# Performance work log

Measured on AMD Instinct MI355X. Metric: run time of the kernel, lower is better.

## Reference

```python
import jax, jax.numpy as jnp
import numpy as np
from jax import lax

B, T, D = 64, 2048, 80
H = 128          # hidden_dim
H2 = 2 * H       # conv out channels / GRU input / bi-GRU output
L = 2            # gru layers
O = 4            # output_dim


def setup_inputs() -> dict:
    key = jax.random.key(0)
    ks = jax.random.split(key, 16)
    f = lambda k, shape, scale: (jax.random.normal(k, shape) * scale).astype(jnp.float32)
    return {
        "x": f(ks[0], (B, T, D), 1.0),
        # conv branches: PyTorch Conv1d weight layout [out, in, k]
        "conv1_w": f(ks[1], (H2, D, 1), 0.1), "conv1_b": f(ks[2], (H2,), 0.1),
        "conv3_w": f(ks[3], (H2, D, 3), 0.06), "conv3_b": f(ks[4], (H2,), 0.1),
        "conv5_w": f(ks[5], (H2, D, 5), 0.05), "conv5_b": f(ks[6], (H2,), 0.1),
        # skip / head linears: PyTorch Linear weight layout [out, in]
        "fc1_w": f(ks[7], (H2, D), 0.1), "fc1_b": f(ks[8], (H2,), 0.1),
        "fc_w": f(ks[9], (O, H2), 0.06), "fc_b": f(ks[10], (O,), 0.1),
        # stacked bidirectional GRU weights: [layer, dir(0=fwd,1=bwd), 3H, ...]
        # gate order along 3H axis follows PyTorch: reset, update, new
        "gru_wih": f(ks[11], (L, 2, 3 * H, H2), 0.06),
        "gru_whh": f(ks[12], (L, 2, 3 * H, H), 0.08),
        "gru_bih": f(ks[13], (L, 2, 3 * H), 0.05),
        "gru_bhh": f(ks[14], (L, 2, 3 * H), 0.05),
    }


def _conv_relu(xc, w, b, pad):
    # xc: [B, C, T], w: [out, in, k]
    y = lax.conv_general_dilated(xc, w, window_strides=(1,), padding=[(pad, pad)],
                                 dimension_numbers=("NCH", "OIH", "NCH"))
    return jax.nn.relu(y + b[None, :, None])


def _gru_dir(xin, wih, whh, bih, bhh, reverse):
    # xin: [B, T, Din]; PyTorch GRU cell: r,z,n gate order
    Hd = whh.shape[1]
    xg = jnp.einsum("btd,gd->btg", xin, wih) + bih  # [B, T, 3H]
    if reverse:
        xg = xg[:, ::-1]

    def step(h, xt):
        hg = h @ whh.T + bhh                                   # [B, 3H]
        r = jax.nn.sigmoid(xt[:, :Hd] + hg[:, :Hd])
        z = jax.nn.sigmoid(xt[:, Hd:2 * Hd] + hg[:, Hd:2 * Hd])
        n = jnp.tanh(xt[:, 2 * Hd:] + r * hg[:, 2 * Hd:])
        hn = (1.0 - z) * n + z * h
        return hn, hn

    h0 = jnp.zeros((xin.shape[0], Hd), xin.dtype)
    _, hs = lax.scan(step, h0, xg.transpose(1, 0, 2))          # [T, B, H]
    hs = hs.transpose(1, 0, 2)
    return hs[:, ::-1] if reverse else hs


def reference(x, conv1_w, conv1_b, conv3_w, conv3_b, conv5_w, conv5_b,
              fc1_w, fc1_b, fc_w, fc_b, gru_wih, gru_whh, gru_bih, gru_bhh):
    xc = x.transpose(0, 2, 1)                                   # [B, D, T]
    oc = (_conv_relu(xc, conv1_w, conv1_b, 0)
          + _conv_relu(xc, conv3_w, conv3_b, 1)
          + _conv_relu(xc, conv5_w, conv5_b, 2))                # [B, 2H, T]
    h = oc.transpose(0, 2, 1)                                   # [B, T, 2H]

    for l in range(gru_wih.shape[0]):
        fwd = _gru_dir(h, gru_wih[l, 0], gru_whh[l, 0], gru_bih[l, 0], gru_bhh[l, 0], False)
        bwd = _gru_dir(h, gru_wih[l, 1], gru_whh[l, 1], gru_bih[l, 1], gru_bhh[l, 1], True)
        h = jnp.concatenate([fwd, bwd], axis=-1)                # [B, T, 2H]

    output_gru = h + x @ fc1_w.T + fc1_b                        # skip connection
    out = output_gru @ fc_w.T + fc_b                            # [B, T, O]
    return output_gru, out
```

## Files before the change

### kernel.cpp

```cpp
#include <hip/hip_runtime.h>
#include <hip/hip_bf16.h>
#include <hip/hip_fp16.h>

typedef _Float16 f16;
typedef _Float16 h2_t __attribute__((ext_vector_type(2)));
typedef _Float16 h4_t __attribute__((ext_vector_type(4)));
typedef _Float16 h8_t __attribute__((ext_vector_type(8)));
typedef float    f4_t __attribute__((ext_vector_type(4)));

#define B_  64
#define T_  2048
#define BT_ 131072
#define OG_ELEMS 33554432ull

__device__ __forceinline__ void gl_lds16(const void* g, void* lds) {
  __builtin_amdgcn_global_load_lds(
      (const __attribute__((address_space(1))) void*)g,
      (__attribute__((address_space(3))) void*)lds, 16, 0, 0);
}

__device__ __forceinline__ h8_t pack8(const float* p) {
  f4_t a = *(const f4_t*)p;
  f4_t b = *(const f4_t*)(p + 4);
  return h8_t{(f16)a[0], (f16)a[1], (f16)a[2], (f16)a[3],
              (f16)b[0], (f16)b[1], (f16)b[2], (f16)b[3]};
}

__device__ __forceinline__ float dpp_swap1(float x) {
  int i = __builtin_bit_cast(int, x);
  int y = __builtin_amdgcn_update_dpp(0, i, 0xB1, 0xF, 0xF, true);
  return __builtin_bit_cast(float, y);
}

__device__ __forceinline__ void kloop128(
    const f16* __restrict__ Ab, int lda,
    const f16* __restrict__ Bb, int ldb,
    int ksteps, f16* As, f16* Bs, f4_t (&acc)[4][4])
{
  const int tid  = threadIdx.x;
  const int wave = tid >> 6, lane = tid & 63;
  const int srow = tid >> 2;
  const int scol = (tid & 3) * 8;
  const int fr   = lane & 15;
  const int kb   = (lane >> 4) * 8;
  const int rA   = (wave >> 1) * 64 + fr;
  const int rB   = (wave & 1) * 64 + fr;

  f16* dA0 = As + wave * 512;
  f16* dA1 = As + 2048 + wave * 512;
  f16* dB0 = Bs + wave * 512;
  f16* dB1 = Bs + 2048 + wave * 512;
  const f16* gA0 = Ab + (size_t)srow * lda + scol;
  const f16* gA1 = Ab + (size_t)(srow + 64) * lda + scol;
  const f16* gB0 = Bb + (size_t)srow * ldb + scol;
  const f16* gB1 = Bb + (size_t)(srow + 64) * ldb + scol;

  for (int kt = 0; kt < ksteps; ++kt) {
    const int ko = kt * 32;
    gl_lds16(gA0 + ko, dA0);
    gl_lds16(gA1 + ko, dA1);
    gl_lds16(gB0 + ko, dB0);
    gl_lds16(gB1 + ko, dB1);
    __syncthreads();
    h8_t af[4], bf[4];
#pragma unroll
    for (int m = 0; m < 4; m++) af[m] = *(const h8_t*)(As + (rA + m * 16) * 32 + kb);
#pragma unroll
    for (int n = 0; n < 4; n++) bf[n] = *(const h8_t*)(Bs + (rB + n * 16) * 32 + kb);
#pragma unroll
    for (int m = 0; m < 4; m++)
#pragma unroll
      for (int n = 0; n < 4; n++)
        acc[m][n] = __builtin_amdgcn_mfma_f32_16x16x32_f16(af[m], bf[n], acc[m][n], 0, 0, 0);
    __syncthreads();
  }
}

__global__ __launch_bounds__(256) void gemm_xT_kernel(
    const f16* __restrict__ A, int lda,
    const f16* __restrict__ Bw, int ldb,
    const float* __restrict__ bias,
    f16* __restrict__ out, int ksteps, int mode)
{
  __shared__ f16 As[4096];
  __shared__ f16 Bs[4096];
  f4_t acc[4][4];
#pragma unroll
  for (int m = 0; m < 4; m++)
#pragma unroll
    for (int n = 0; n < 4; n++) acc[m][n] = f4_t{0.f, 0.f, 0.f, 0.f};

  const f16* Ab = A + (size_t)blockIdx.x * 128 * lda;
  const f16* Bb = Bw + (size_t)blockIdx.y * 128 * ldb;
  kloop128(Ab, lda, Bb, ldb, ksteps, As, Bs, acc);

  const int tid = threadIdx.x, wave = tid >> 6, lane = tid & 63;
  const int col0 = blockIdx.y * 128 + (wave & 1) * 64 + (lane & 15);
  const int row0 = blockIdx.x * 128 + (wave >> 1) * 64 + (lane >> 4) * 4;
  const int b = blockIdx.x >> 4;
#pragma unroll
  for (int n = 0; n < 4; n++) {
    const int col = col0 + n * 16;
    const float bv = bias[col];
    const int g = col >> 7, jj = col & 127;
    const size_t base = (mode == 0)
        ? ((size_t)((b * 3 + g) * 128 + jj)) * 2048
        : ((size_t)((g * 64 + b) * 128 + jj)) * 2048;
#pragma unroll
    for (int m = 0; m < 4; m++) {
      const int row = row0 + m * 16;
      const int t = row & 2047;
      h4_t v = h4_t{(f16)(acc[m][n][0] + bv), (f16)(acc[m][n][1] + bv),
                    (f16)(acc[m][n][2] + bv), (f16)(acc[m][n][3] + bv)};
      *(h4_t*)(out + base + t) = v;
    }
  }
}

__global__ __launch_bounds__(256) void conv3sum_kernel(
    const f16* __restrict__ A5,
    const f16* __restrict__ W5p, const f16* __restrict__ W3p, const f16* __restrict__ W1p,
    const float* __restrict__ b5, const float* __restrict__ b3, const float* __restrict__ b1,
    f16* __restrict__ oc)
{
  __shared__ f16 As[4096];
  __shared__ f16 Bs[4096];
  const int tid = threadIdx.x, wave = tid >> 6, lane = tid & 63;
  const int col0 = blockIdx.y * 128 + (wave & 1) * 64 + (lane & 15);
  const int row0 = blockIdx.x * 128 + (wave >> 1) * 64 + (lane >> 4) * 4;
  const f16* Ab = A5 + (size_t)blockIdx.x * 128 * 480;

  f4_t tot[4][4];
#pragma unroll
  for (int m = 0; m < 4; m++)
#pragma unroll
    for (int n = 0; n < 4; n++) tot[m][n] = f4_t{0.f, 0.f, 0.f, 0.f};

  auto seg = [&](const f16* Wp, int ldb, int ks, int aoff, const float* bias) {
    f4_t acc[4][4];
#pragma unroll
    for (int m = 0; m < 4; m++)
#pragma unroll
      for (int n = 0; n < 4; n++) acc[m][n] = f4_t{0.f, 0.f, 0.f, 0.f};
    kloop128(Ab + aoff, 480, Wp + (size_t)blockIdx.y * 128 * ldb, ldb, ks, As, Bs, acc);
#pragma unroll
    for (int n = 0; n < 4; n++) {
      const float bv = bias[col0 + n * 16];
#pragma unroll
      for (int m = 0; m < 4; m++)
#pragma unroll
        for (int q = 0; q < 4; q++)
          tot[m][n][q] += fmaxf(acc[m][n][q] + bv, 0.f);
    }
  };
  seg(W5p, 480, 15, 0,   b5);
  seg(W3p, 288, 9,  96,  b3);
  seg(W1p, 96,  3,  192, b1);

#pragma unroll
  for (int n = 0; n < 4; n++) {
    const int col = col0 + n * 16;
#pragma unroll
    for (int m = 0; m < 4; m++) {
      const int row = row0 + m * 16;
#pragma unroll
      for (int q = 0; q < 4; q++)
        oc[(size_t)(row + q) * 256 + col] = (f16)tot[m][n][q];
    }
  }
}

__global__ __launch_bounds__(384) void im2col_kernel(
    const float* __restrict__ x, f16* __restrict__ A5)
{
  const int tid = threadIdx.x;
  const int r = tid / 12, c8 = tid % 12;
  const int bt = blockIdx.x * 32 + r;
  const int kg = blockIdx.y;
  const int b = bt >> 11, t = bt & 2047;
  const int ts = t + kg - 2;
  h8_t v = {0, 0, 0, 0, 0, 0, 0, 0};
  if (c8 < 10 && (unsigned)ts < 2048u) {
    const float* src = x + ((size_t)(b << 11) + ts) * 80 + c8 * 8;
    f4_t a = *(const f4_t*)src;
    f4_t bvec = *(const f4_t*)(src + 4);
    v = h8_t{(f16)a[0], (f16)a[1], (f16)a[2], (f16)a[3],
             (f16)bvec[0], (f16)bvec[1], (f16)bvec[2], (f16)bvec[3]};
  }
  *(h8_t*)(A5 + (size_t)bt * 480 + kg * 96 + c8 * 8) = v;
}

__global__ void pack_convw_kernel(
    const float* __restrict__ w1, const float* __restrict__ w3,
    const float* __restrict__ w5, const float* __restrict__ fc1w,
    f16* __restrict__ W5p, f16* __restrict__ W3p, f16* __restrict__ W1p,
    f16* __restrict__ FC1p)
{
  const int col = blockIdx.x;
  const int c = threadIdx.x;
  if (col < 480) {
    const int kg = col / 96, d = col % 96;
    W5p[c * 480 + col] = (f16)((d < 80) ? w5[(c * 80 + d) * 5 + kg] : 0.f);
  } else if (col < 768) {
    const int cc = col - 480, k = cc / 96, d = cc % 96;
    W3p[c * 288 + cc] = (f16)((d < 80) ? w3[(c * 80 + d) * 3 + k] : 0.f);
  } else if (col < 864) {
    const int d = col - 768;
    W1p[c * 96 + d] = (f16)((d < 80) ? w1[c * 80 + d] : 0.f);
  } else {
    const int d = col - 864;
    FC1p[c * 96 + d] = (f16)((d < 80) ? fc1w[c * 80 + d] : 0.f);
  }
}

__global__ void cast_f16_kernel(const float* __restrict__ src, f16* __restrict__ dst, int n8)
{
  const int i = blockIdx.x * blockDim.x + threadIdx.x;
  if (i >= n8) return;
  f4_t a = *(const f4_t*)(src + (size_t)i * 8);
  f4_t b = *(const f4_t*)(src + (size_t)i * 8 + 4);
  h8_t v = h8_t{(f16)a[0], (f16)a[1], (f16)a[2], (f16)a[3],
                (f16)b[0], (f16)b[1], (f16)b[2], (f16)b[3]};
  *(h8_t*)(dst + (size_t)i * 8) = v;
}

__device__ __forceinline__ float fastrcp(float x)  { return __builtin_amdgcn_rcpf(x); }
__device__ __forceinline__ float fastex2(float x)  { return __builtin_amdgcn_exp2f(x); }

#define DOT8(acc0, acc1, hv, wv)                                                       \
  do {                                                                                 \
    acc0 = __builtin_amdgcn_fdot2(h2_t{hv[0], hv[1]}, h2_t{wv[0], wv[1]}, acc0, false);\
    acc1 = __builtin_amdgcn_fdot2(h2_t{hv[2], hv[3]}, h2_t{wv[2], wv[3]}, acc1, false);\
    acc0 = __builtin_amdgcn_fdot2(h2_t{hv[4], hv[5]}, h2_t{wv[4], wv[5]}, acc0, false);\
    acc1 = __builtin_amdgcn_fdot2(h2_t{hv[6], hv[7]}, h2_t{wv[6], wv[7]}, acc1, false);\
  } while (0)

template<int DIR, int L1>
__device__ __forceinline__ void gru_chain(
    const f16* __restrict__ xg_b,
    const f16* __restrict__ xf_b,
    const f16* __restrict__ whh_d,
    const float* __restrict__ bhh_d,
    f16* __restrict__ h0_b,
    float* __restrict__ og_b)
{
  const int tid  = threadIdx.x;
  const int wv   = tid >> 6;
  const int lane = tid & 63;
  const int j    = wv * 32 + (lane >> 1);
  const int kh   = lane & 1;

  h8_t WR[8], WZ[8], WN[8];
  {
    const int co = kh * 64;
#pragma unroll
    for (int q = 0; q < 8; q++) WR[q] = *(const h8_t*)(whh_d + (size_t)j * 128 + co + q * 8);
#pragma unroll
    for (int q = 0; q < 8; q++) WZ[q] = *(const h8_t*)(whh_d + (size_t)(128 + j) * 128 + co + q * 8);
#pragma unroll
    for (int q = 0; q < 8; q++) WN[q] = *(const h8_t*)(whh_d + (size_t)(256 + j) * 128 + co + q * 8);
  }
#pragma unroll
  for (int q = 0; q < 8; q++) {
    asm volatile("" : "+v"(WR[q]), "+v"(WZ[q]), "+v"(WN[q]));
  }
  float br = bhh_d[j], bz = bhh_d[128 + j], bn = bhh_d[256 + j];
  asm volatile("" : "+v"(br), "+v"(bz), "+v"(bn));

  __shared__ __align__(16) f16 hb[2][128];
  if (tid < 128) { hb[0][tid] = (f16)0.f; hb[1][tid] = (f16)0.f; }
  float hstate = 0.f;

  h8_t xrA{}, xzA{}, xnA{}, xfA{};
  h8_t xrB{}, xzB{}, xnB{}, xfB{};
  auto ld4 = [&](int s8, h8_t& xr, h8_t& xz, h8_t& xn, h8_t& xf) {
    const int tb = DIR ? (T_ - 8 - s8) : s8;
    xr = *(const h8_t*)(xg_b + (size_t)(0 * 128 + j) * 2048 + tb);
    xz = *(const h8_t*)(xg_b + (size_t)(1 * 128 + j) * 2048 + tb);
    xn = *(const h8_t*)(xg_b + (size_t)(2 * 128 + j) * 2048 + tb);
    if (L1) xf = *(const h8_t*)(xf_b + (size_t)j * 2048 + tb);
  };
  ld4(0, xrA, xzA, xnA, xfA);
  asm volatile("s_waitcnt lgkmcnt(0)" ::: "memory");
  __builtin_amdgcn_s_barrier();
  __builtin_amdgcn_sched_barrier(0);

  for (int s8 = 0; s8 < T_; s8 += 8) {
    if ((s8 + 8) < T_) ld4(s8 + 8, xrB, xzB, xnB, xfB);
#pragma unroll
    for (int ss = 0; ss < 8; ss++) {
      const int e = DIR ? (7 - ss) : ss;
      const f16* hbuf = &hb[ss & 1][0] + kh * 64;
      h8_t hv[8];
#pragma unroll
      for (int q = 0; q < 8; q++) hv[q] = *(const h8_t*)(hbuf + q * 8);
      float r0 = 0.f, r1 = 0.f, z0 = 0.f, z1 = 0.f, n0 = 0.f, n1 = 0.f;
#pragma unroll
      for (int q = 0; q < 8; q++) {
        DOT8(r0, r1, hv[q], WR[q]);
        DOT8(z0, z1, hv[q], WZ[q]);
        DOT8(n0, n1, hv[q], WN[q]);
      }
      float sr = r0 + r1; sr += dpp_swap1(sr);
      float sz = z0 + z1; sz += dpp_swap1(sz);
      float sn = n0 + n1; sn += dpp_swap1(sn);
      const float rr = fastrcp(1.f + fastex2(((float)xrA[e] + sr + br) * -1.44269504f));
      const float zz = fastrcp(1.f + fastex2(((float)xzA[e] + sz + bz) * -1.44269504f));
      const float na = (float)xnA[e] + rr * (sn + bn);
      const float ex = fastex2(fabsf(na) * 2.88539008f);
      const float th = copysignf(1.f - 2.f * fastrcp(ex + 1.f), na);
      hstate = (1.f - zz) * th + zz * hstate;
      const int t = DIR ? (T_ - 1 - (s8 + ss)) : (s8 + ss);
      if (!kh) {
        if (L1) og_b[(size_t)t * 256 + j] = hstate + (float)xfA[e];
        else    h0_b[(size_t)t * 256 + j] = (f16)hstate;
        hb[(ss & 1) ^ 1][j] = (f16)hstate;
      }
      asm volatile("s_waitcnt lgkmcnt(0)" ::: "memory");
      __builtin_amdgcn_s_barrier();
      __builtin_amdgcn_sched_barrier(0);
    }
    xrA = xrB; xzA = xzB; xnA = xnB;
    if (L1) xfA = xfB;
  }
}

__global__ __launch_bounds__(256, 1) void gru_rec7_kernel(
    const f16* __restrict__ xgT, const f16* __restrict__ whhp,
    const float* __restrict__ bhh, const f16* __restrict__ xfT,
    f16* __restrict__ h0out, float* __restrict__ ogout)
{
  const int b = blockIdx.x >> 1, d = blockIdx.x & 1;
  const f16* xg_b = xgT + (size_t)(d * 64 + b) * 3 * 128 * 2048;
  const f16* xf_b = xfT ? (xfT + (size_t)(d * 64 + b) * 128 * 2048) : nullptr;
  const f16* whh_d = whhp + (size_t)d * 384 * 128;
  const float* bhh_d = bhh + d * 384;
  f16* h0_b = h0out ? (h0out + (size_t)b * 2048 * 256 + d * 128) : nullptr;
  float* og_b = ogout ? (ogout + (size_t)b * 2048 * 256 + d * 128) : nullptr;

  if (ogout) {
    if (d == 0) gru_chain<0, 1>(xg_b, xf_b, whh_d, bhh_d, nullptr, og_b);
    else        gru_chain<1, 1>(xg_b, xf_b, whh_d, bhh_d, nullptr, og_b);
  } else {
    if (d == 0) gru_chain<0, 0>(xg_b, nullptr, whh_d, bhh_d, h0_b, nullptr);
    else        gru_chain<1, 0>(xg_b, nullptr, whh_d, bhh_d, h0_b, nullptr);
  }
}

__global__ __launch_bounds__(256) void fc_out_kernel(
    const float* __restrict__ og, const float* __restrict__ fcw,
    const float* __restrict__ fcb, float* __restrict__ out)
{
  const int lane = threadIdx.x & 63;
  const int wid = (blockIdx.x * 256 + threadIdx.x) >> 6;
  const int nw = (gridDim.x * 256) >> 6;
  const f4_t w0 = *(const f4_t*)(fcw + 0 * 256 + lane * 4);
  const f4_t w1 = *(const f4_t*)(fcw + 1 * 256 + lane * 4);
  const f4_t w2 = *(const f4_t*)(fcw + 2 * 256 + lane * 4);
  const f4_t w3 = *(const f4_t*)(fcw + 3 * 256 + lane * 4);
  const float b0 = fcb[0], b1 = fcb[1], b2 = fcb[2], b3 = fcb[3];
  for (int row = wid; row < BT_; row += nw) {
    const f4_t v = *(const f4_t*)(og + (size_t)row * 256 + lane * 4);
    float p0 = v[0] * w0[0] + v[1] * w0[1] + v[2] * w0[2] + v[3] * w0[3];
    float p1 = v[0] * w1[0] + v[1] * w1[1] + v[2] * w1[2] + v[3] * w1[3];
    float p2 = v[0] * w2[0] + v[1] * w2[1] + v[2] * w2[2] + v[3] * w2[3];
    float p3 = v[0] * w3[0] + v[1] * w3[1] + v[2] * w3[2] + v[3] * w3[3];
#pragma unroll
    for (int off = 1; off < 64; off <<= 1) {
      p0 += __shfl_xor(p0, off);
      p1 += __shfl_xor(p1, off);
      p2 += __shfl_xor(p2, off);
      p3 += __shfl_xor(p3, off);
    }
    if (lane == 0) {
      f4_t o4 = f4_t{p0 + b0, p1 + b1, p2 + b2, p3 + b3};
      *(f4_t*)(out + (size_t)row * 4) = o4;
    }
  }
}

extern "C" void kernel_launch(void* const* d_in, const int* in_sizes, int n_in,
                              void* d_out, int out_size, void* d_ws, size_t ws_size,
                              hipStream_t stream)
{
  const float* x       = (const float*)d_in[0];
  const float* conv1_w = (const float*)d_in[1];
  const float* conv1_b = (const float*)d_in[2];
  const float* conv3_w = (const float*)d_in[3];
  const float* conv3_b = (const float*)d_in[4];
  const float* conv5_w = (const float*)d_in[5];
  const float* conv5_b = (const float*)d_in[6];
  const float* fc1_w   = (const float*)d_in[7];
  const float* fc1_b   = (const float*)d_in[8];
  const float* fc_w    = (const float*)d_in[9];
  const float* fc_b    = (const float*)d_in[10];
  const float* gru_wih = (const float*)d_in[11];
  const float* gru_whh = (const float*)d_in[12];
  const float* gru_bih = (const float*)d_in[13];
  const float* gru_bhh = (const float*)d_in[14];

  size_t off = 0;
  auto alloc = [&](size_t bytes) {
    char* p = (char*)d_ws + off;
    off += (bytes + 255) & ~(size_t)255;
    return p;
  };
  f16* A5   = (f16*)alloc((size_t)BT_ * 480 * 2);
  f16* W5p  = (f16*)alloc(256 * 480 * 2);
  f16* W3p  = (f16*)alloc(256 * 288 * 2);
  f16* W1p  = (f16*)alloc(256 * 96 * 2);
  f16* FC1p = (f16*)alloc(256 * 96 * 2);
  f16* wihp = (f16*)alloc(4ull * 384 * 256 * 2);
  f16* whhp = (f16*)alloc(4ull * 384 * 128 * 2);
  f16* oc   = (f16*)alloc((size_t)BT_ * 256 * 2);
  f16* xgT  = (f16*)alloc(2ull * 64 * 3 * 128 * 2048 * 2);
  f16* h0   = (f16*)alloc((size_t)BT_ * 256 * 2);
  f16* xfT  = (f16*)alloc(2ull * 64 * 128 * 2048 * 2);
  if (off > ws_size) return;

  float* og   = (float*)d_out;
  float* out2 = (float*)d_out + OG_ELEMS;

  im2col_kernel<<<dim3(BT_ / 32, 5), 384, 0, stream>>>(x, A5);
  pack_convw_kernel<<<960, 256, 0, stream>>>(conv1_w, conv3_w, conv5_w, fc1_w,
                                             W5p, W3p, W1p, FC1p);
  cast_f16_kernel<<<(49152 + 255) / 256, 256, 0, stream>>>(gru_wih, wihp, 49152);
  cast_f16_kernel<<<(24576 + 255) / 256, 256, 0, stream>>>(gru_whh, whhp, 24576);

  conv3sum_kernel<<<dim3(1024, 2), 256, 0, stream>>>(A5, W5p, W3p, W1p,
                                                     conv5_b, conv3_b, conv1_b, oc);
  gemm_xT_kernel<<<dim3(1024, 2), 256, 0, stream>>>(A5 + 192, 480, FC1p, 96,
                                                    fc1_b, xfT, 3, 1);

  for (int l = 0; l < 2; ++l) {
    const f16* hin = l ? h0 : oc;
    for (int d = 0; d < 2; ++d) {
      gemm_xT_kernel<<<dim3(1024, 3), 256, 0, stream>>>(
          hin, 256, wihp + (size_t)(l * 2 + d) * 384 * 256, 256,
          gru_bih + (l * 2 + d) * 384,
          xgT + (size_t)d * 64 * 3 * 128 * 2048, 8, 0);
    }
    gru_rec7_kernel<<<128, 256, 0, stream>>>(
        xgT, whhp + (size_t)l * 2 * 384 * 128, gru_bhh + (size_t)l * 2 * 384,
        l ? xfT : nullptr, l ? nullptr : h0, l ? og : nullptr);
  }

  fc_out_kernel<<<1024, 256, 0, stream>>>(og, fc_w, fc_b, out2);
}
```

Before: 2.185 ms.

## Process two batch sequences per GRU recurrence block to share barriers

The recurrent GRU kernel now has each workgroup advance two independent batch sequences in lockstep with shared register-resident weights. This halves the grid to 64 blocks. The aim is to amortize per-timestep LDS barrier and latency overhead across two chains and give the scheduler independent work to interleave. The cost is double the arithmetic per step on the serial path and fewer active CUs.

```diff
diff --git a/kernel.cpp b/kernel.cpp
--- a/kernel.cpp
+++ b/kernel.cpp
@@ -236,114 +236,156 @@
   } while (0)
 
 template<int DIR, int L1>
-__device__ __forceinline__ void gru_chain(
-    const f16* __restrict__ xg_b,
-    const f16* __restrict__ xf_b,
+__device__ __forceinline__ void gru_chain8(
+    const f16* __restrict__ xgA, const f16* __restrict__ xgB,
+    const f16* __restrict__ xfA_, const f16* __restrict__ xfB_,
     const f16* __restrict__ whh_d,
     const float* __restrict__ bhh_d,
-    f16* __restrict__ h0_b,
-    float* __restrict__ og_b)
+    f16* __restrict__ h0A, f16* __restrict__ h0B,
+    float* __restrict__ ogA, float* __restrict__ ogB)
 {
   const int tid  = threadIdx.x;
   const int wv   = tid >> 6;
   const int lane = tid & 63;
   const int j    = wv * 32 + (lane >> 1);
   const int kh   = lane & 1;
+  const int co   = kh * 64;
 
   h8_t WR[8], WZ[8], WN[8];
-  {
-    const int co = kh * 64;
-#pragma unroll
-    for (int q = 0; q < 8; q++) WR[q] = *(const h8_t*)(whh_d + (size_t)j * 128 + co + q * 8);
-#pragma unroll
-    for (int q = 0; q < 8; q++) WZ[q] = *(const h8_t*)(whh_d + (size_t)(128 + j) * 128 + co + q * 8);
-#pragma unroll
-    for (int q = 0; q < 8; q++) WN[q] = *(const h8_t*)(whh_d + (size_t)(256 + j) * 128 + co + q * 8);
-  }
-#pragma unroll
-  for (int q = 0; q < 8; q++) {
-    asm volatile("" : "+v"(WR[q]), "+v"(WZ[q]), "+v"(WN[q]));
-  }
-  float br = bhh_d[j], bz = bhh_d[128 + j], bn = bhh_d[256 + j];
-  asm volatile("" : "+v"(br), "+v"(bz), "+v"(bn));
-
-  __shared__ __align__(16) f16 hb[2][128];
-  if (tid < 128) { hb[0][tid] = (f16)0.f; hb[1][tid] = (f16)0.f; }
-  float hstate = 0.f;
-
-  h8_t xrA{}, xzA{}, xnA{}, xfA{};
-  h8_t xrB{}, xzB{}, xnB{}, xfB{};
-  auto ld4 = [&](int s8, h8_t& xr, h8_t& xz, h8_t& xn, h8_t& xf) {
+#pragma unroll
+  for (int q = 0; q < 8; q++) WR[q] = *(const h8_t*)(whh_d + (size_t)j * 128 + co + q * 8);
+#pragma unroll
+  for (int q = 0; q < 8; q++) WZ[q] = *(const h8_t*)(whh_d + (size_t)(128 + j) * 128 + co + q * 8);
+#pragma unroll
+  for (int q = 0; q < 8; q++) WN[q] = *(const h8_t*)(whh_d + (size_t)(256 + j) * 128 + co + q * 8);
+  const float br = bhh_d[j], bz = bhh_d[128 + j], bn = bhh_d[256 + j];
+
+  __shared__ __align__(16) f16 hbA[2][128];
+  __shared__ __align__(16) f16 hbB[2][128];
+  if (tid < 128) {
+    hbA[0][tid] = (f16)0.f; hbA[1][tid] = (f16)0.f;
+    hbB[0][tid] = (f16)0.f; hbB[1][tid] = (f16)0.f;
+  }
+  float hsA = 0.f, hsB = 0.f;
+
+  h8_t xrA0{}, xzA0{}, xnA0{}, xfA0{}, xrA1{}, xzA1{}, xnA1{}, xfA1{};
+  h8_t xrB0{}, xzB0{}, xnB0{}, xfB0{}, xrB1{}, xzB1{}, xnB1{}, xfB1{};
+  auto ld4 = [&](const f16* xg_b, const f16* xf_b, int s8,
+                 h8_t& xr, h8_t& xz, h8_t& xn, h8_t& xf) {
     const int tb = DIR ? (T_ - 8 - s8) : s8;
     xr = *(const h8_t*)(xg_b + (size_t)(0 * 128 + j) * 2048 + tb);
     xz = *(const h8_t*)(xg_b + (size_t)(1 * 128 + j) * 2048 + tb);
     xn = *(const h8_t*)(xg_b + (size_t)(2 * 128 + j) * 2048 + tb);
     if (L1) xf = *(const h8_t*)(xf_b + (size_t)j * 2048 + tb);
   };
-  ld4(0, xrA, xzA, xnA, xfA);
+  ld4(xgA, xfA_, 0, xrA0, xzA0, xnA0, xfA0);
+  ld4(xgB, xfB_, 0, xrB0, xzB0, xnB0, xfB0);
   asm volatile("s_waitcnt lgkmcnt(0)" ::: "memory");
   __builtin_amdgcn_s_barrier();
   __builtin_amdgcn_sched_barrier(0);
 
   for (int s8 = 0; s8 < T_; s8 += 8) {
-    if ((s8 + 8) < T_) ld4(s8 + 8, xrB, xzB, xnB, xfB);
+#pragma unroll
+    for (int q = 0; q < 8; q++) {
+      asm volatile("" : "+v"(WR[q]), "+v"(WZ[q]), "+v"(WN[q]));
+    }
+    if ((s8 + 8) < T_) {
+      ld4(xgA, xfA_, s8 + 8, xrA1, xzA1, xnA1, xfA1);
+      ld4(xgB, xfB_, s8 + 8, xrB1, xzB1, xnB1, xfB1);
+    }
 #pragma unroll
     for (int ss = 0; ss < 8; ss++) {
       const int e = DIR ? (7 - ss) : ss;
-      const f16* hbuf = &hb[ss & 1][0] + kh * 64;
-      h8_t hv[8];
-#pragma unroll
-      for (int q = 0; q < 8; q++) hv[q] = *(const h8_t*)(hbuf + q * 8);
-      float r0 = 0.f, r1 = 0.f, z0 = 0.f, z1 = 0.f, n0 = 0.f, n1 = 0.f;
+      const int t = DIR ? (T_ - 1 - (s8 + ss)) : (s8 + ss);
+      const f16* hbufA = &hbA[ss & 1][0] + co;
+      const f16* hbufB = &hbB[ss & 1][0] + co;
+      h8_t hvA[8], hvB[8];
+#pragma unroll
+      for (int q = 0; q < 8; q++) hvA[q] = *(const h8_t*)(hbufA + q * 8);
+#pragma unroll
+      for (int q = 0; q < 8; q++) hvB[q] = *(const h8_t*)(hbufB + q * 8);
+      float rA0 = 0.f, rA1 = 0.f, zA0 = 0.f, zA1 = 0.f, nA0 = 0.f, nA1 = 0.f;
 #pragma unroll
       for (int q = 0; q < 8; q++) {
-        DOT8(r0, r1, hv[q], WR[q]);
-        DOT8(z0, z1, hv[q], WZ[q]);
-        DOT8(n0, n1, hv[q], WN[q]);
+        DOT8(rA0, rA1, hvA[q], WR[q]);
+        DOT8(zA0, zA1, hvA[q], WZ[q]);
+        DOT8(nA0, nA1, hvA[q], WN[q]);
       }
-      float sr = r0 + r1; sr += dpp_swap1(sr);
-      float sz = z0 + z1; sz += dpp_swap1(sz);
-      float sn = n0 + n1; sn += dpp_swap1(sn);
-      const float rr = fastrcp(1.f + fastex2(((float)xrA[e] + sr + br) * -1.44269504f));
-      const float zz = fastrcp(1.f + fastex2(((float)xzA[e] + sz + bz) * -1.44269504f));
-      const float na = (float)xnA[e] + rr * (sn + bn);
-      const float ex = fastex2(fabsf(na) * 2.88539008f);
-      const float th = copysignf(1.f - 2.f * fastrcp(ex + 1.f), na);
-      hstate = (1.f - zz) * th + zz * hstate;
-      const int t = DIR ? (T_ - 1 - (s8 + ss)) : (s8 + ss);
-      if (!kh) {
-        if (L1) og_b[(size_t)t * 256 + j] = hstate + (float)xfA[e];
-        else    h0_b[(size_t)t * 256 + j] = (f16)hstate;
-        hb[(ss & 1) ^ 1][j] = (f16)hstate;
+      float rB0 = 0.f, rB1 = 0.f, zB0 = 0.f, zB1 = 0.f, nB0 = 0.f, nB1 = 0.f;
+#pragma unroll
+      for (int q = 0; q < 8; q++) {
+        DOT8(rB0, rB1, hvB[q], WR[q]);
+        DOT8(zB0, zB1, hvB[q], WZ[q]);
+        DOT8(nB0, nB1, hvB[q], WN[q]);
+      }
+      float srA = rA0 + rA1; srA += dpp_swap1(srA);
+      float szA = zA0 + zA1; szA += dpp_swap1(szA);
+      float snA = nA0 + nA1; snA += dpp_swap1(snA);
+      {
+        const float rr = fastrcp(1.f + fastex2(((float)xrA0[e] + srA + br) * -1.44269504f));
+        const float zz = fastrcp(1.f + fastex2(((float)xzA0[e] + szA + bz) * -1.44269504f));
+        const float na = (float)xnA0[e] + rr * (snA + bn);
+        const float ex = fastex2(fabsf(na) * 2.88539008f);
+        const float th = copysignf(1.f - 2.f * fastrcp(ex + 1.f), na);
+        hsA = (1.f - zz) * th + zz * hsA;
+        if (!kh) {
+          if (L1) ogA[(size_t)t * 256 + j] = hsA + (float)xfA0[e];
+          else    h0A[(size_t)t * 256 + j] = (f16)hsA;
+          hbA[(ss & 1) ^ 1][j] = (f16)hsA;
+        }
+      }
+      float srB = rB0 + rB1; srB += dpp_swap1(srB);
+      float szB = zB0 + zB1; szB += dpp_swap1(szB);
+      float snB = nB0 + nB1; snB += dpp_swap1(snB);
+      {
+        const float rr = fastrcp(1.f + fastex2(((float)xrB0[e] + srB + br) * -1.44269504f));
+        const float zz = fastrcp(1.f + fastex2(((float)xzB0[e] + szB + bz) * -1.44269504f));
+        const float na = (float)xnB0[e] + rr * (snB + bn);
+        const float ex = fastex2(fabsf(na) * 2.88539008f);
+        const float th = copysignf(1.f - 2.f * fastrcp(ex + 1.f), na);
+        hsB = (1.f - zz) * th + zz * hsB;
+        if (!kh) {
+          if (L1) ogB[(size_t)t * 256 + j] = hsB + (float)xfB0[e];
+          else    h0B[(size_t)t * 256 + j] = (f16)hsB;
+          hbB[(ss & 1) ^ 1][j] = (f16)hsB;
+        }
       }
       asm volatile("s_waitcnt lgkmcnt(0)" ::: "memory");
       __builtin_amdgcn_s_barrier();
       __builtin_amdgcn_sched_barrier(0);
     }
-    xrA = xrB; xzA = xzB; xnA = xnB;
-    if (L1) xfA = xfB;
-  }
-}
-
-__global__ __launch_bounds__(256, 1) void gru_rec7_kernel(
+    xrA0 = xrA1; xzA0 = xzA1; xnA0 = xnA1;
+    xrB0 = xrB1; xzB0 = xzB1; xnB0 = xnB1;
+    if (L1) { xfA0 = xfA1; xfB0 = xfB1; }
+  }
+}
+
+__global__ __launch_bounds__(256, 1) void gru_rec8_kernel(
     const f16* __restrict__ xgT, const f16* __restrict__ whhp,
     const float* __restrict__ bhh, const f16* __restrict__ xfT,
     f16* __restrict__ h0out, float* __restrict__ ogout)
 {
-  const int b = blockIdx.x >> 1, d = blockIdx.x & 1;
-  const f16* xg_b = xgT + (size_t)(d * 64 + b) * 3 * 128 * 2048;
-  const f16* xf_b = xfT ? (xfT + (size_t)(d * 64 + b) * 128 * 2048) : nullptr;
+  const int d  = blockIdx.x & 1;
+  const int bp = blockIdx.x >> 1;
+  const int bA = 2 * bp, bB = 2 * bp + 1;
+
+  const f16* xgA = xgT + (size_t)(d * 64 + bA) * 786432;
+  const f16* xgB = xgT + (size_t)(d * 64 + bB) * 786432;
+  const f16* xfA = xfT ? (xfT + (size_t)(d * 64 + bA) * 262144) : nullptr;
+  const f16* xfB = xfT ? (xfT + (size_t)(d * 64 + bB) * 262144) : nullptr;
   const f16* whh_d = whhp + (size_t)d * 384 * 128;
   const float* bhh_d = bhh + d * 384;
-  f16* h0_b = h0out ? (h0out + (size_t)b * 2048 * 256 + d * 128) : nullptr;
-  float* og_b = ogout ? (ogout + (size_t)b * 2048 * 256 + d * 128) : nullptr;
+  f16* h0A = h0out ? (h0out + (size_t)bA * 524288 + d * 128) : nullptr;
+  f16* h0B = h0out ? (h0out + (size_t)bB * 524288 + d * 128) : nullptr;
+  float* ogA = ogout ? (ogout + (size_t)bA * 524288 + d * 128) : nullptr;
+  float* ogB = ogout ? (ogout + (size_t)bB * 524288 + d * 128) : nullptr;
 
   if (ogout) {
-    if (d == 0) gru_chain<0, 1>(xg_b, xf_b, whh_d, bhh_d, nullptr, og_b);
-    else        gru_chain<1, 1>(xg_b, xf_b, whh_d, bhh_d, nullptr, og_b);
+    if (d == 0) gru_chain8<0, 1>(xgA, xgB, xfA, xfB, whh_d, bhh_d, nullptr, nullptr, ogA, ogB);
+    else        gru_chain8<1, 1>(xgA, xgB, xfA, xfB, whh_d, bhh_d, nullptr, nullptr, ogA, ogB);
   } else {
-    if (d == 0) gru_chain<0, 0>(xg_b, nullptr, whh_d, bhh_d, h0_b, nullptr);
-    else        gru_chain<1, 0>(xg_b, nullptr, whh_d, bhh_d, h0_b, nullptr);
+    if (d == 0) gru_chain8<0, 0>(xgA, xgB, nullptr, nullptr, whh_d, bhh_d, h0A, h0B, nullptr, nullptr);
+    else        gru_chain8<1, 0>(xgA, xgB, nullptr, nullptr, whh_d, bhh_d, h0A, h0B, nullptr, nullptr);
   }
 }
 
@@ -440,7 +482,7 @@
           gru_bih + (l * 2 + d) * 384,
           xgT + (size_t)d * 64 * 3 * 128 * 2048, 8, 0);
     }
-    gru_rec7_kernel<<<128, 256, 0, stream>>>(
+    gru_rec8_kernel<<<64, 256, 0, stream>>>(
         xgT, whhp + (size_t)l * 2 * 384 * 128, gru_bhh + (size_t)l * 2 * 384,
         l ? xfT : nullptr, l ? nullptr : h0, l ? og : nullptr);
   }
```

After: 3.597 ms. 1.65x slower.
